# Optimization experiments

Measured on AMD Instinct MI355X. Metric: run time of the kernel, lower is better.

Reference implementation:

```python
import jax, jax.numpy as jnp
import numpy as np

UNITS = 1024
D_MODEL = 1024
H = 16
DK = 64
DV = 64
M = 128
B = 4
S = 1024


def setup_inputs() -> dict:
    key = jax.random.key(0)
    ks = jax.random.split(key, 12)
    s = 1.0 / np.sqrt(D_MODEL)
    inp = {
        "queries": jax.random.normal(ks[0], (B, S, D_MODEL), jnp.float32),
        "keys": jax.random.normal(ks[1], (B, S, D_MODEL), jnp.float32),
        "values": jax.random.normal(ks[2], (B, S, D_MODEL), jnp.float32),
        "Wq": jax.random.normal(ks[3], (D_MODEL, H * DK), jnp.float32) * s,
        "bq": jnp.zeros((H * DK,), jnp.float32),
        "Wk": jax.random.normal(ks[4], (D_MODEL, H * DK), jnp.float32) * s,
        "bk": jnp.zeros((H * DK,), jnp.float32),
        "Wv": jax.random.normal(ks[5], (D_MODEL, H * DV), jnp.float32) * s,
        "bv": jnp.zeros((H * DV,), jnp.float32),
        "Wo": jax.random.normal(ks[6], (H * DV, UNITS), jnp.float32) * (1.0 / np.sqrt(H * DV)),
        "bo": jnp.zeros((UNITS,), jnp.float32),
        "mk": jax.random.normal(ks[7], (1, M, H * DK), jnp.float32) * 0.1,
        "mv": jax.random.normal(ks[8], (1, M, H * DV), jnp.float32) * 0.1,
        "h": H,
    }
    return inp


def reference(queries, keys, values, Wq, bq, Wk, bk, Wv, bv, Wo, bo, mk, mv, h):
    Bq, Sq, _ = queries.shape
    m = mk.shape[1]
    dk = Wk.shape[1] // h
    dv = Wv.shape[1] // h
    scale_m = jnp.sqrt(jnp.asarray(m, queries.dtype))

    # Q projection: [B, h, Sq, dk]
    q = (queries @ Wq + bq).reshape(Bq, Sq, h, dk).transpose(0, 2, 1, 3)

    # K/V projections with m learned memory slots concatenated on the seq axis
    k_flat = jnp.concatenate(
        [keys @ Wk + bk, scale_m * jnp.broadcast_to(mk, (Bq, m, h * dk))], axis=1
    )  # [B, Sk+m, h*dk]
    v_flat = jnp.concatenate(
        [values @ Wv + bv, scale_m * jnp.broadcast_to(mv, (Bq, m, h * dv))], axis=1
    )  # [B, Sk+m, h*dv]
    Skm = k_flat.shape[1]
    k = k_flat.reshape(Bq, Skm, h, dk).transpose(0, 2, 1, 3)  # [B, h, Sk+m, dk]
    v = v_flat.reshape(Bq, Skm, h, dv).transpose(0, 2, 1, 3)  # [B, h, Sk+m, dv]

    # Scaled dot-product attention over sequence + memory slots
    scores = jnp.einsum("bhqd,bhkd->bhqk", q, k) / jnp.sqrt(jnp.asarray(dk, q.dtype))
    attn = jax.nn.softmax(scores, axis=-1)  # [B, h, Sq, Sk+m]
    out = jnp.einsum("bhqk,bhkd->bhqd", attn, v)  # [B, h, Sq, dv]
    out = out.transpose(0, 2, 1, 3).reshape(Bq, Sq, h * dv)
    return out @ Wo + bo
```

## Files before the change

kernel.cpp:

```cpp
#include <hip/hip_runtime.h>

typedef __attribute__((ext_vector_type(8))) __bf16 bf16x8;
typedef __attribute__((ext_vector_type(4))) float f32x4;

#define DEVINL __device__ __forceinline__

constexpr int BZ = 4;
constexpr int SEQ = 1024;
constexpr int DMODEL = 1024;
constexpr int NH = 16;
constexpr int HD = 64;
constexpr int MSLOT = 128;
constexpr int NT = BZ * SEQ;
constexpr int SKM = SEQ + MSLOT;
constexpr int VT_LD = BZ * SKM;
constexpr float SCALE_M = 11.313708498984761f;
constexpr float SCEXP = 0.18033688011112042f;
constexpr size_t OF_QIN  = 0;
constexpr size_t OF_KIN  = OF_QIN  + (size_t)NT * DMODEL;
constexpr size_t OF_VIN  = OF_KIN  + (size_t)NT * DMODEL;
constexpr size_t OF_WQT  = OF_VIN  + (size_t)NT * DMODEL;
constexpr size_t OF_WKT  = OF_WQT  + (size_t)DMODEL * DMODEL;
constexpr size_t OF_WVT  = OF_WKT  + (size_t)DMODEL * DMODEL;
constexpr size_t OF_WOT  = OF_WVT  + (size_t)DMODEL * DMODEL;
constexpr size_t OF_QB   = OF_WOT  + (size_t)DMODEL * DMODEL;
constexpr size_t OF_KPR  = OF_QB   + (size_t)NT * DMODEL;
constexpr size_t OF_KMEM = OF_KPR  + (size_t)NT * DMODEL;
constexpr size_t OF_VTG  = OF_KMEM + (size_t)MSLOT * DMODEL;
constexpr size_t OF_AOUT = OF_VTG  + (size_t)DMODEL * VT_LD;

DEVINL unsigned short f2bf(float f) {
  union { float f; unsigned u; } v; v.f = f;
  unsigned r = v.u + 0x7FFF + ((v.u >> 16) & 1);
  return (unsigned short)(r >> 16);
}

#if __has_builtin(__builtin_amdgcn_cvt_pk_bf16_f32)
DEVINL unsigned pack2(float a, float b) {
  auto t = __builtin_amdgcn_cvt_pk_bf16_f32(a, b);
  unsigned r; __builtin_memcpy(&r, &t, 4); return r;
}
#else
DEVINL unsigned pack2(float a, float b) {
  return (unsigned)f2bf(a) | ((unsigned)f2bf(b) << 16);
}
#endif

#if __has_builtin(__builtin_amdgcn_exp2f)
DEVINL float fast_exp2(float x) { return __builtin_amdgcn_exp2f(x); }
#else
DEVINL float fast_exp2(float x) { return exp2f(x); }
#endif

DEVINL f32x4 mfma16(bf16x8 a, bf16x8 b, f32x4 c) {
  return __builtin_amdgcn_mfma_f32_16x16x32_bf16(a, b, c, 0, 0, 0);
}

DEVINL void gload16(const unsigned short* gp, unsigned short* lp) {
  __builtin_amdgcn_global_load_lds(
      (const __attribute__((address_space(1))) unsigned int*)(const void*)gp,
      (__attribute__((address_space(3))) unsigned int*)(void*)lp, 16, 0, 0);
}


__global__ __launch_bounds__(256) void cvt3_bf16(const float* __restrict__ q,
                                                 const float* __restrict__ k,
                                                 const float* __restrict__ v,
                                                 unsigned short* __restrict__ dq,
                                                 unsigned short* __restrict__ dk,
                                                 unsigned short* __restrict__ dv) {
  const float* src = (blockIdx.y == 0) ? q : (blockIdx.y == 1) ? k : v;
  unsigned short* dst = (blockIdx.y == 0) ? dq : (blockIdx.y == 1) ? dk : dv;
  int i = (blockIdx.x * 256 + threadIdx.x) * 8;
  float4 v0 = *(const float4*)(src + i);
  float4 v1 = *(const float4*)(src + i + 4);
  union { unsigned u2[4]; uint4 v; } o;
  o.u2[0] = pack2(v0.x, v0.y); o.u2[1] = pack2(v0.z, v0.w);
  o.u2[2] = pack2(v1.x, v1.y); o.u2[3] = pack2(v1.z, v1.w);
  *(uint4*)(dst + i) = o.v;
}

__global__ __launch_bounds__(256) void transpose_cvt4(
    const float* __restrict__ s0, const float* __restrict__ s1,
    const float* __restrict__ s2, const float* __restrict__ s3,
    unsigned short* __restrict__ d0, unsigned short* __restrict__ d1,
    unsigned short* __restrict__ d2, unsigned short* __restrict__ d3) {
  const float* src = (blockIdx.z == 0) ? s0 : (blockIdx.z == 1) ? s1 : (blockIdx.z == 2) ? s2 : s3;
  unsigned short* dst = (blockIdx.z == 0) ? d0 : (blockIdx.z == 1) ? d1 : (blockIdx.z == 2) ? d2 : d3;
  __shared__ float t[32][65];
  const int tid = threadIdx.x;
  const int n0 = blockIdx.x * 32, k0 = blockIdx.y * 64;
  {
    int c = tid & 31, rg = tid >> 5;
#pragma unroll
    for (int rr = 0; rr < 8; ++rr)
      t[c][rg * 8 + rr] = src[(size_t)(k0 + rg * 8 + rr) * DMODEL + n0 + c];
  }
  __syncthreads();
  {
    int n = tid >> 3, ck = tid & 7;
    union { unsigned short u[8]; uint4 v; } o;
#pragma unroll
    for (int j = 0; j < 8; ++j) o.u[j] = f2bf(t[n][ck * 8 + j]);
    *(uint4*)(dst + (size_t)(n0 + n) * DMODEL + k0 + ck * 8) = o.v;
  }
}

__global__ __launch_bounds__(256) void kmem_cvt(const float* __restrict__ mk,
                                                unsigned short* __restrict__ dst) {
  int i = blockIdx.x * 256 + threadIdx.x;
  dst[i] = f2bf(mk[i] * SCALE_M);
}

__global__ __launch_bounds__(256) void vmem_transpose(const float* __restrict__ mv,
                                                      unsigned short* __restrict__ VtG) {
  __shared__ float t[32][33];
  const int tx = threadIdx.x, ty = threadIdx.y;
  const int j0 = blockIdx.x * 32, c0 = blockIdx.y * 32;
#pragma unroll
  for (int r = 0; r < 4; ++r)
    t[ty + r * 8][tx] = mv[(size_t)(j0 + ty + r * 8) * DMODEL + c0 + tx];
  __syncthreads();
#pragma unroll
  for (int r = 0; r < 4; ++r) {
    int c = c0 + ty + r * 8;
    unsigned short v = f2bf(t[tx][ty + r * 8] * SCALE_M);
#pragma unroll
    for (int bb = 0; bb < BZ; ++bb)
      VtG[(size_t)c * VT_LD + bb * SKM + SEQ + j0 + tx] = v;
  }
}


DEVINL void gemm_stage(const unsigned short* big, const unsigned short* sm,
                       unsigned short* B0, unsigned short* B1,
                       unsigned short* S0, unsigned short* S1,
                       int k0, int tid) {
#pragma unroll
  for (int hb = 0; hb < 2; ++hb) {
    unsigned short* bl = hb ? B1 : B0;
#pragma unroll
    for (int gi = 0; gi < 2; ++gi) {
      int g = gi * 256 + tid;
      int row = g >> 2, slot = g & 3;
      gload16(big + (size_t)row * DMODEL + k0 + hb * 32 + slot * 8, bl + g * 8);
    }
    unsigned short* sl = hb ? S1 : S0;
    int row = tid >> 2, slot = tid & 3;
    gload16(sm + (size_t)row * DMODEL + k0 + hb * 32 + slot * 8, sl + tid * 8);
  }
}

DEVINL void gemm_compute(const unsigned short* B0, const unsigned short* B1,
                         const unsigned short* S0, const unsigned short* S1,
                         int wr, int wc, int quad, int l16, f32x4 acc[4][2]) {
#pragma unroll
  for (int hb = 0; hb < 2; ++hb) {
    const unsigned short* bl = hb ? B1 : B0;
    const unsigned short* sl = hb ? S1 : S0;
    bf16x8 af[4], bfr[2];
#pragma unroll
    for (int rb = 0; rb < 4; ++rb)
      af[rb] = *(const bf16x8*)(bl + (wr * 64 + rb * 16 + l16) * 32 + quad * 8);
#pragma unroll
    for (int cb = 0; cb < 2; ++cb)
      bfr[cb] = *(const bf16x8*)(sl + (wc * 32 + cb * 16 + l16) * 32 + quad * 8);
#pragma unroll
    for (int rb = 0; rb < 4; ++rb)
#pragma unroll
      for (int cb = 0; cb < 2; ++cb)
        acc[rb][cb] = mfma16(af[rb], bfr[cb], acc[rb][cb]);
  }
}

__global__ __launch_bounds__(256) void proj_qkv(
    const unsigned short* __restrict__ Qin, const unsigned short* __restrict__ Kin,
    const unsigned short* __restrict__ Vin, const unsigned short* __restrict__ Wqt,
    const unsigned short* __restrict__ Wkt, const unsigned short* __restrict__ Wvt,
    const float* __restrict__ bq, const float* __restrict__ bk,
    const float* __restrict__ bv, unsigned short* __restrict__ Qbp,
    unsigned short* __restrict__ Kprp, unsigned short* __restrict__ VtG) {
  __shared__ unsigned short Big0[128 * 32], Big1[128 * 32];
  __shared__ unsigned short Sm0[64 * 32], Sm1[64 * 32];
  const int tid = threadIdx.x;
  const int pid = blockIdx.x >> 9;
  const int idx = blockIdx.x & 511;
  const int w = tid >> 6, lane = tid & 63, quad = lane >> 4, l16 = lane & 15;
  const int wr = w >> 1, wc = w & 1;
  f32x4 acc[4][2] = {};

  if (pid < 2) {
    const unsigned short* A  = pid ? Kin : Qin;
    const unsigned short* Wt = pid ? Wkt : Wqt;
    const float* bias        = pid ? bk : bq;
    unsigned short* out      = pid ? Kprp : Qbp;
    const int n0 = (idx & 15) * 64, m0 = (idx >> 4) * 128;
    const unsigned short* big = A + (size_t)m0 * DMODEL;
    const unsigned short* sm  = Wt + (size_t)n0 * DMODEL;
    for (int kt = 0; kt < 16; ++kt) {
      gemm_stage(big, sm, Big0, Big1, Sm0, Sm1, kt * 64, tid);
      __syncthreads();
      gemm_compute(Big0, Big1, Sm0, Sm1, wr, wc, quad, l16, acc);
      __syncthreads();
    }
#pragma unroll
    for (int rb = 0; rb < 4; ++rb)
#pragma unroll
      for (int cb = 0; cb < 2; ++cb)
#pragma unroll
        for (int r = 0; r < 4; ++r) {
          int row = m0 + wr * 64 + rb * 16 + quad * 4 + r;
          int col = n0 + wc * 32 + cb * 16 + l16;
          out[(size_t)row * DMODEL + col] = f2bf(acc[rb][cb][r] + bias[col]);
        }
  } else {
    const int t0 = (idx & 63) * 64, n0 = (idx >> 6) * 128;
    const unsigned short* big = Wvt + (size_t)n0 * DMODEL;
    const unsigned short* sm  = Vin + (size_t)t0 * DMODEL;
    for (int kt = 0; kt < 16; ++kt) {
      gemm_stage(big, sm, Big0, Big1, Sm0, Sm1, kt * 64, tid);
      __syncthreads();
      gemm_compute(Big0, Big1, Sm0, Sm1, wr, wc, quad, l16, acc);
      __syncthreads();
    }
#pragma unroll
    for (int rb = 0; rb < 4; ++rb)
#pragma unroll
      for (int cb = 0; cb < 2; ++cb)
#pragma unroll
        for (int r = 0; r < 4; ++r) {
          int n = n0 + wr * 64 + rb * 16 + quad * 4 + r;
          int tok = t0 + wc * 32 + cb * 16 + l16;
          int col = tok + (tok >> 10) * MSLOT;
          VtG[(size_t)n * VT_LD + col] = f2bf(acc[rb][cb][r] + bv[n]);
        }
  }
}

__global__ __launch_bounds__(256) void gemm_out(const unsigned short* __restrict__ A,
                                                const unsigned short* __restrict__ Wt,
                                                const float* __restrict__ bias,
                                                float* __restrict__ Cout) {
  __shared__ unsigned short As[128 * 32];
  __shared__ unsigned short Bs[64 * 32];
  const int tid = threadIdx.x;
  const int m0 = blockIdx.y * 128;
  const int n0 = blockIdx.x * 64;
  const int w = tid >> 6, lane = tid & 63, quad = lane >> 4, l16 = lane & 15;
  const int wr = w >> 1, wc = w & 1;
  f32x4 acc[4][2] = {};
  for (int kt = 0; kt < 32; ++kt) {
    const int k0 = kt * 32;
#pragma unroll
    for (int gi = 0; gi < 2; ++gi) {
      int g = gi * 256 + tid;
      int row = g >> 2, slot = g & 3;
      gload16(A + (size_t)(m0 + row) * DMODEL + k0 + slot * 8, As + g * 8);
    }
    {
      int row = tid >> 2, slot = tid & 3;
      gload16(Wt + (size_t)(n0 + row) * DMODEL + k0 + slot * 8, Bs + tid * 8);
    }
    __syncthreads();
    bf16x8 af[4], bfr[2];
#pragma unroll
    for (int rb = 0; rb < 4; ++rb)
      af[rb] = *(const bf16x8*)(As + (wr * 64 + rb * 16 + l16) * 32 + quad * 8);
#pragma unroll
    for (int cb = 0; cb < 2; ++cb)
      bfr[cb] = *(const bf16x8*)(Bs + (wc * 32 + cb * 16 + l16) * 32 + quad * 8);
#pragma unroll
    for (int rb = 0; rb < 4; ++rb)
#pragma unroll
      for (int cb = 0; cb < 2; ++cb)
        acc[rb][cb] = mfma16(af[rb], bfr[cb], acc[rb][cb]);
    __syncthreads();
  }
#pragma unroll
  for (int rb = 0; rb < 4; ++rb)
#pragma unroll
    for (int cb = 0; cb < 2; ++cb)
#pragma unroll
      for (int r = 0; r < 4; ++r) {
        int row = m0 + wr * 64 + rb * 16 + quad * 4 + r;
        int col = n0 + wc * 32 + cb * 16 + l16;
        Cout[(size_t)row * DMODEL + col] = acc[rb][cb][r] + bias[col];
      }
}

__global__ __launch_bounds__(256) void attn_kernel(const unsigned short* __restrict__ Qb,
                                                   const unsigned short* __restrict__ Kproj,
                                                   const unsigned short* __restrict__ Kmem,
                                                   const unsigned short* __restrict__ VtG,
                                                   unsigned short* __restrict__ Aout) {
  __shared__ unsigned short Ks[64 * 72];
  __shared__ unsigned short Vs[64 * 72];
  __shared__ unsigned short Pl[4 * 32 * 72];
  const int tid = threadIdx.x;
  const int qb = blockIdx.x, h = blockIdx.y, b = blockIdx.z;
  const int w = tid >> 6, lane = tid & 63, quad = lane >> 4, l16 = lane & 15;
  const int token0 = b * SEQ + qb * 128 + w * 32;
  unsigned short* Pw = Pl + w * 32 * 72;

  const int row0 = tid >> 3, slot0 = tid & 7;
  const int g1 = tid + 256;
  const int row1 = g1 >> 3, slot1 = g1 & 7;

  auto kbase = [&](int tile) -> const unsigned short* {
    return (tile < 16) ? Kproj + (size_t)(b * SEQ + tile * 64) * DMODEL + h * HD
                       : Kmem + (size_t)((tile - 16) * 64) * DMODEL + h * HD;
  };
  auto vbase = [&](int tile) -> const unsigned short* {
    int c0 = (tile < 16) ? b * SKM + tile * 64 : b * SKM + SEQ + (tile - 16) * 64;
    return VtG + (size_t)(h * HD) * VT_LD + c0;
  };

  bf16x8 qf[2][2];
#pragma unroll
  for (int g = 0; g < 2; ++g)
#pragma unroll
    for (int t = 0; t < 2; ++t)
      qf[g][t] = *(const bf16x8*)(Qb + (size_t)(token0 + g * 16 + l16) * DMODEL +
                                  h * HD + t * 32 + quad * 8);

  f32x4 O[2][4] = {};
  float lsum[2] = {0.0f, 0.0f};

  uint4 kr0, kr1, vr0, vr1;
  {
    const unsigned short* kp = kbase(0);
    const unsigned short* vp = vbase(0);
    kr0 = *(const uint4*)(kp + (size_t)row0 * DMODEL + slot0 * 8);
    kr1 = *(const uint4*)(kp + (size_t)row1 * DMODEL + slot1 * 8);
    vr0 = *(const uint4*)(vp + (size_t)row0 * VT_LD + slot0 * 8);
    vr1 = *(const uint4*)(vp + (size_t)row1 * VT_LD + slot1 * 8);
  }

  for (int tile = 0; tile < 18; ++tile) {
    *(uint4*)(Ks + row0 * 72 + slot0 * 8) = kr0;
    *(uint4*)(Ks + row1 * 72 + slot1 * 8) = kr1;
    *(uint4*)(Vs + row0 * 72 + slot0 * 8) = vr0;
    *(uint4*)(Vs + row1 * 72 + slot1 * 8) = vr1;
    __syncthreads();
    if (tile < 17) {
      const unsigned short* kp = kbase(tile + 1);
      const unsigned short* vp = vbase(tile + 1);
      kr0 = *(const uint4*)(kp + (size_t)row0 * DMODEL + slot0 * 8);
      kr1 = *(const uint4*)(kp + (size_t)row1 * DMODEL + slot1 * 8);
      vr0 = *(const uint4*)(vp + (size_t)row0 * VT_LD + slot0 * 8);
      vr1 = *(const uint4*)(vp + (size_t)row1 * VT_LD + slot1 * 8);
    }

#pragma unroll
    for (int g = 0; g < 2; ++g) {
      f32x4 sc[4] = {};
#pragma unroll
      for (int c = 0; c < 4; ++c)
#pragma unroll
        for (int t = 0; t < 2; ++t) {
          bf16x8 kb = *(const bf16x8*)(Ks + (c * 16 + l16) * 72 + t * 32 + quad * 8);
          sc[c] = mfma16(kb, qf[g][t], sc[c]);
        }
#pragma unroll
      for (int c = 0; c < 4; ++c) {
        float p0 = fast_exp2(sc[c][0] * SCEXP);
        float p1 = fast_exp2(sc[c][1] * SCEXP);
        float p2 = fast_exp2(sc[c][2] * SCEXP);
        float p3 = fast_exp2(sc[c][3] * SCEXP);
        lsum[g] += (p0 + p1) + (p2 + p3);
        union { unsigned u[2]; } pk;
        pk.u[0] = pack2(p0, p1);
        pk.u[1] = pack2(p2, p3);
        *(uint2*)(Pw + (g * 16 + l16) * 72 + c * 16 + quad * 4) = *(uint2*)pk.u;
      }
    }
    __builtin_amdgcn_wave_barrier();

#pragma unroll
    for (int t2 = 0; t2 < 2; ++t2) {
      bf16x8 pa0 = *(const bf16x8*)(Pw + (0 + l16) * 72 + t2 * 32 + quad * 8);
      bf16x8 pa1 = *(const bf16x8*)(Pw + (16 + l16) * 72 + t2 * 32 + quad * 8);
#pragma unroll
      for (int c2 = 0; c2 < 4; ++c2) {
        bf16x8 vb = *(const bf16x8*)(Vs + (c2 * 16 + l16) * 72 + t2 * 32 + quad * 8);
        O[0][c2] = mfma16(pa0, vb, O[0][c2]);
        O[1][c2] = mfma16(pa1, vb, O[1][c2]);
      }
    }
    __syncthreads();
  }

#pragma unroll
  for (int g = 0; g < 2; ++g) {
    float ls = lsum[g];
    ls += __shfl_xor(ls, 16);
    ls += __shfl_xor(ls, 32);
#pragma unroll
    for (int r = 0; r < 4; ++r) {
      float lv = __shfl(ls, quad * 4 + r, 16);
      float inv = 1.0f / lv;
#pragma unroll
      for (int c2 = 0; c2 < 4; ++c2)
        Aout[(size_t)(token0 + g * 16 + quad * 4 + r) * DMODEL + h * HD + c2 * 16 + l16] =
            f2bf(O[g][c2][r] * inv);
    }
  }
}

extern "C" void kernel_launch(void* const* d_in, const int* in_sizes, int n_in,
                              void* d_out, int out_size, void* d_ws, size_t ws_size,
                              hipStream_t stream) {
  const float* queries = (const float*)d_in[0];
  const float* keys    = (const float*)d_in[1];
  const float* values  = (const float*)d_in[2];
  const float* Wq = (const float*)d_in[3];
  const float* bq = (const float*)d_in[4];
  const float* Wk = (const float*)d_in[5];
  const float* bk = (const float*)d_in[6];
  const float* Wv = (const float*)d_in[7];
  const float* bv = (const float*)d_in[8];
  const float* Wo = (const float*)d_in[9];
  const float* bo = (const float*)d_in[10];
  const float* mk = (const float*)d_in[11];
  const float* mv = (const float*)d_in[12];

  unsigned short* ws = (unsigned short*)d_ws;
  unsigned short* Qin  = ws + OF_QIN;
  unsigned short* Kin  = ws + OF_KIN;
  unsigned short* Vin  = ws + OF_VIN;
  unsigned short* Wqt  = ws + OF_WQT;
  unsigned short* Wkt  = ws + OF_WKT;
  unsigned short* Wvt  = ws + OF_WVT;
  unsigned short* Wot  = ws + OF_WOT;
  unsigned short* Qbp  = ws + OF_QB;
  unsigned short* Kprp = ws + OF_KPR;
  unsigned short* Kmm  = ws + OF_KMEM;
  unsigned short* VtGp = ws + OF_VTG;
  unsigned short* Aoutp = ws + OF_AOUT;

  cvt3_bf16<<<dim3(2048, 3), 256, 0, stream>>>(queries, keys, values, Qin, Kin, Vin);

  transpose_cvt4<<<dim3(32, 16, 4), 256, 0, stream>>>(Wq, Wk, Wv, Wo, Wqt, Wkt, Wvt, Wot);

  kmem_cvt<<<(MSLOT * DMODEL) / 256, 256, 0, stream>>>(mk, Kmm);
  vmem_transpose<<<dim3(MSLOT / 32, DMODEL / 32), dim3(32, 8), 0, stream>>>(mv, VtGp);

  proj_qkv<<<1536, 256, 0, stream>>>(Qin, Kin, Vin, Wqt, Wkt, Wvt, bq, bk, bv,
                                     Qbp, Kprp, VtGp);

  attn_kernel<<<dim3(8, 16, 4), 256, 0, stream>>>(Qbp, Kprp, Kmm, VtGp, Aoutp);

  gemm_out<<<dim3(16, 32), 256, 0, stream>>>(Aoutp, Wot, bo, (float*)d_out);
}
```

Baseline: 231.9 us.

## Merge prep kernels into one launch, reuse staged GEMM in out projection, remap attention grid

Fuses the four preprocessing kernels (activation conversion, weight transpose, memory key/value conversion) into a single launch dispatched by block index, which removes three kernel launches and their gaps. The output GEMM now reuses the proj_qkv gemm_stage/gemm_compute helpers with a 64-wide K step and two LDS halves, halving the number of barrier pairs. The attention grid is flattened to 1D with (b,h) in the low bits so neighbouring blocks cover different heads and batches, which changes L2 locality. The branchy fused kernel sizes every block's shared memory for the weight transpose, and the new GEMM needs more LDS.

```diff
diff --git a/kernel.cpp b/kernel.cpp
--- a/kernel.cpp
+++ b/kernel.cpp
@@ -62,72 +62,69 @@
       (__attribute__((address_space(3))) unsigned int*)(void*)lp, 16, 0, 0);
 }
 
-
-__global__ __launch_bounds__(256) void cvt3_bf16(const float* __restrict__ q,
-                                                 const float* __restrict__ k,
-                                                 const float* __restrict__ v,
-                                                 unsigned short* __restrict__ dq,
-                                                 unsigned short* __restrict__ dk,
-                                                 unsigned short* __restrict__ dv) {
-  const float* src = (blockIdx.y == 0) ? q : (blockIdx.y == 1) ? k : v;
-  unsigned short* dst = (blockIdx.y == 0) ? dq : (blockIdx.y == 1) ? dk : dv;
-  int i = (blockIdx.x * 256 + threadIdx.x) * 8;
-  float4 v0 = *(const float4*)(src + i);
-  float4 v1 = *(const float4*)(src + i + 4);
-  union { unsigned u2[4]; uint4 v; } o;
-  o.u2[0] = pack2(v0.x, v0.y); o.u2[1] = pack2(v0.z, v0.w);
-  o.u2[2] = pack2(v1.x, v1.y); o.u2[3] = pack2(v1.z, v1.w);
-  *(uint4*)(dst + i) = o.v;
-}
-
-__global__ __launch_bounds__(256) void transpose_cvt4(
-    const float* __restrict__ s0, const float* __restrict__ s1,
-    const float* __restrict__ s2, const float* __restrict__ s3,
+__global__ __launch_bounds__(256) void prep_all(
+    const float* __restrict__ q, const float* __restrict__ k, const float* __restrict__ v,
+    const float* __restrict__ W0, const float* __restrict__ W1,
+    const float* __restrict__ W2, const float* __restrict__ W3,
+    const float* __restrict__ mk, const float* __restrict__ mv,
+    unsigned short* __restrict__ dq, unsigned short* __restrict__ dk,
+    unsigned short* __restrict__ dv,
     unsigned short* __restrict__ d0, unsigned short* __restrict__ d1,
-    unsigned short* __restrict__ d2, unsigned short* __restrict__ d3) {
-  const float* src = (blockIdx.z == 0) ? s0 : (blockIdx.z == 1) ? s1 : (blockIdx.z == 2) ? s2 : s3;
-  unsigned short* dst = (blockIdx.z == 0) ? d0 : (blockIdx.z == 1) ? d1 : (blockIdx.z == 2) ? d2 : d3;
+    unsigned short* __restrict__ d2, unsigned short* __restrict__ d3,
+    unsigned short* __restrict__ Kmm, unsigned short* __restrict__ VtG) {
   __shared__ float t[32][65];
   const int tid = threadIdx.x;
-  const int n0 = blockIdx.x * 32, k0 = blockIdx.y * 64;
-  {
-    int c = tid & 31, rg = tid >> 5;
-#pragma unroll
-    for (int rr = 0; rr < 8; ++rr)
-      t[c][rg * 8 + rr] = src[(size_t)(k0 + rg * 8 + rr) * DMODEL + n0 + c];
-  }
-  __syncthreads();
-  {
-    int n = tid >> 3, ck = tid & 7;
-    union { unsigned short u[8]; uint4 v; } o;
-#pragma unroll
-    for (int j = 0; j < 8; ++j) o.u[j] = f2bf(t[n][ck * 8 + j]);
-    *(uint4*)(dst + (size_t)(n0 + n) * DMODEL + k0 + ck * 8) = o.v;
-  }
-}
-
-__global__ __launch_bounds__(256) void kmem_cvt(const float* __restrict__ mk,
-                                                unsigned short* __restrict__ dst) {
-  int i = blockIdx.x * 256 + threadIdx.x;
-  dst[i] = f2bf(mk[i] * SCALE_M);
-}
-
-__global__ __launch_bounds__(256) void vmem_transpose(const float* __restrict__ mv,
-                                                      unsigned short* __restrict__ VtG) {
-  __shared__ float t[32][33];
-  const int tx = threadIdx.x, ty = threadIdx.y;
-  const int j0 = blockIdx.x * 32, c0 = blockIdx.y * 32;
-#pragma unroll
-  for (int r = 0; r < 4; ++r)
-    t[ty + r * 8][tx] = mv[(size_t)(j0 + ty + r * 8) * DMODEL + c0 + tx];
-  __syncthreads();
-#pragma unroll
-  for (int r = 0; r < 4; ++r) {
-    int c = c0 + ty + r * 8;
-    unsigned short v = f2bf(t[tx][ty + r * 8] * SCALE_M);
-#pragma unroll
-    for (int bb = 0; bb < BZ; ++bb)
-      VtG[(size_t)c * VT_LD + bb * SKM + SEQ + j0 + tx] = v;
+  const int bid = blockIdx.x;
+  if (bid < 6144) {
+    const int tz = bid >> 11;
+    const float* src = (tz == 0) ? q : (tz == 1) ? k : v;
+    unsigned short* dst = (tz == 0) ? dq : (tz == 1) ? dk : dv;
+    int i = ((bid & 2047) * 256 + tid) * 8;
+    float4 v0 = *(const float4*)(src + i);
+    float4 v1 = *(const float4*)(src + i + 4);
+    union { unsigned u2[4]; uint4 v; } o;
+    o.u2[0] = pack2(v0.x, v0.y); o.u2[1] = pack2(v0.z, v0.w);
+    o.u2[2] = pack2(v1.x, v1.y); o.u2[3] = pack2(v1.z, v1.w);
+    *(uint4*)(dst + i) = o.v;
+  } else if (bid < 8192) {
+    const int rel = bid - 6144;
+    const int z = rel >> 9, rem = rel & 511;
+    const float* src = (z == 0) ? W0 : (z == 1) ? W1 : (z == 2) ? W2 : W3;
+    unsigned short* dst = (z == 0) ? d0 : (z == 1) ? d1 : (z == 2) ? d2 : d3;
+    const int n0 = (rem & 31) * 32, k0 = (rem >> 5) * 64;
+    {
+      int c = tid & 31, rg = tid >> 5;
+#pragma unroll
+      for (int rr = 0; rr < 8; ++rr)
+        t[c][rg * 8 + rr] = src[(size_t)(k0 + rg * 8 + rr) * DMODEL + n0 + c];
+    }
+    __syncthreads();
+    {
+      int n = tid >> 3, ck = tid & 7;
+      union { unsigned short u[8]; uint4 v; } o;
+#pragma unroll
+      for (int j = 0; j < 8; ++j) o.u[j] = f2bf(t[n][ck * 8 + j]);
+      *(uint4*)(dst + (size_t)(n0 + n) * DMODEL + k0 + ck * 8) = o.v;
+    }
+  } else if (bid < 8704) {
+    int i = (bid - 8192) * 256 + tid;
+    Kmm[i] = f2bf(mk[i] * SCALE_M);
+  } else {
+    const int rel = bid - 8704;
+    const int j0 = (rel & 3) * 32, c0 = (rel >> 2) * 32;
+    const int tx = tid & 31, ty = tid >> 5;
+#pragma unroll
+    for (int r = 0; r < 4; ++r)
+      t[ty + r * 8][tx] = mv[(size_t)(j0 + ty + r * 8) * DMODEL + c0 + tx];
+    __syncthreads();
+#pragma unroll
+    for (int r = 0; r < 4; ++r) {
+      int c = c0 + ty + r * 8;
+      unsigned short vv = f2bf(t[tx][ty + r * 8] * SCALE_M);
+#pragma unroll
+      for (int bb = 0; bb < BZ; ++bb)
+        VtG[(size_t)c * VT_LD + bb * SKM + SEQ + j0 + tx] = vv;
+    }
   }
 }
 
@@ -241,39 +238,20 @@
                                                 const unsigned short* __restrict__ Wt,
                                                 const float* __restrict__ bias,
                                                 float* __restrict__ Cout) {
-  __shared__ unsigned short As[128 * 32];
-  __shared__ unsigned short Bs[64 * 32];
+  __shared__ unsigned short Big0[128 * 32], Big1[128 * 32];
+  __shared__ unsigned short Sm0[64 * 32], Sm1[64 * 32];
   const int tid = threadIdx.x;
-  const int m0 = blockIdx.y * 128;
-  const int n0 = blockIdx.x * 64;
+  const int idx = blockIdx.x;
+  const int n0 = (idx & 15) * 64, m0 = (idx >> 4) * 128;
   const int w = tid >> 6, lane = tid & 63, quad = lane >> 4, l16 = lane & 15;
   const int wr = w >> 1, wc = w & 1;
   f32x4 acc[4][2] = {};
-  for (int kt = 0; kt < 32; ++kt) {
-    const int k0 = kt * 32;
-#pragma unroll
-    for (int gi = 0; gi < 2; ++gi) {
-      int g = gi * 256 + tid;
-      int row = g >> 2, slot = g & 3;
-      gload16(A + (size_t)(m0 + row) * DMODEL + k0 + slot * 8, As + g * 8);
-    }
-    {
-      int row = tid >> 2, slot = tid & 3;
-      gload16(Wt + (size_t)(n0 + row) * DMODEL + k0 + slot * 8, Bs + tid * 8);
-    }
-    __syncthreads();
-    bf16x8 af[4], bfr[2];
-#pragma unroll
-    for (int rb = 0; rb < 4; ++rb)
-      af[rb] = *(const bf16x8*)(As + (wr * 64 + rb * 16 + l16) * 32 + quad * 8);
-#pragma unroll
-    for (int cb = 0; cb < 2; ++cb)
-      bfr[cb] = *(const bf16x8*)(Bs + (wc * 32 + cb * 16 + l16) * 32 + quad * 8);
-#pragma unroll
-    for (int rb = 0; rb < 4; ++rb)
-#pragma unroll
-      for (int cb = 0; cb < 2; ++cb)
-        acc[rb][cb] = mfma16(af[rb], bfr[cb], acc[rb][cb]);
+  const unsigned short* big = A + (size_t)m0 * DMODEL;
+  const unsigned short* sm  = Wt + (size_t)n0 * DMODEL;
+  for (int kt = 0; kt < 16; ++kt) {
+    gemm_stage(big, sm, Big0, Big1, Sm0, Sm1, kt * 64, tid);
+    __syncthreads();
+    gemm_compute(Big0, Big1, Sm0, Sm1, wr, wc, quad, l16, acc);
     __syncthreads();
   }
 #pragma unroll
@@ -297,7 +275,8 @@
   __shared__ unsigned short Vs[64 * 72];
   __shared__ unsigned short Pl[4 * 32 * 72];
   const int tid = threadIdx.x;
-  const int qb = blockIdx.x, h = blockIdx.y, b = blockIdx.z;
+  const int bh = blockIdx.x & 63, qb = blockIdx.x >> 6;
+  const int b = bh & 3, h = bh >> 2;
   const int w = tid >> 6, lane = tid & 63, quad = lane >> 4, l16 = lane & 15;
   const int token0 = b * SEQ + qb * 128 + w * 32;
   unsigned short* Pw = Pl + w * 32 * 72;
@@ -438,17 +417,13 @@
   unsigned short* VtGp = ws + OF_VTG;
   unsigned short* Aoutp = ws + OF_AOUT;
 
-  cvt3_bf16<<<dim3(2048, 3), 256, 0, stream>>>(queries, keys, values, Qin, Kin, Vin);
-
-  transpose_cvt4<<<dim3(32, 16, 4), 256, 0, stream>>>(Wq, Wk, Wv, Wo, Wqt, Wkt, Wvt, Wot);
-
-  kmem_cvt<<<(MSLOT * DMODEL) / 256, 256, 0, stream>>>(mk, Kmm);
-  vmem_transpose<<<dim3(MSLOT / 32, DMODEL / 32), dim3(32, 8), 0, stream>>>(mv, VtGp);
+  prep_all<<<8832, 256, 0, stream>>>(queries, keys, values, Wq, Wk, Wv, Wo, mk, mv,
+                                     Qin, Kin, Vin, Wqt, Wkt, Wvt, Wot, Kmm, VtGp);
 
   proj_qkv<<<1536, 256, 0, stream>>>(Qin, Kin, Vin, Wqt, Wkt, Wvt, bq, bk, bv,
                                      Qbp, Kprp, VtGp);
 
-  attn_kernel<<<dim3(8, 16, 4), 256, 0, stream>>>(Qbp, Kprp, Kmm, VtGp, Aoutp);
-
-  gemm_out<<<dim3(16, 32), 256, 0, stream>>>(Aoutp, Wot, bo, (float*)d_out);
-}
+  attn_kernel<<<512, 256, 0, stream>>>(Qbp, Kprp, Kmm, VtGp, Aoutp);
+
+  gemm_out<<<512, 256, 0, stream>>>(Aoutp, Wot, bo, (float*)d_out);
+}
```

Measured after the change: 222.2 us. 1.04x faster.
